# Kernel optimization log

Hardware: AMD Instinct MI355X
Metric: run time of the kernel (lower is better)

Reference implementation:

```python
import jax, jax.numpy as jnp
import numpy as np

DIM = 256
NUM_HEADS = 8
RATIO = 4
K_SAMPLES = 2
B, C, H, W = 2, 256, 64, 64


def setup_inputs() -> dict:
    key = jax.random.key(0)
    ks = jax.random.split(key, 12)
    N_low = (H // RATIO) * (W // RATIO)
    s = 0.02
    return {
        "q_high_feat": jax.random.normal(ks[0], (B, C, H, W), dtype=jnp.float32),
        "k_high_feat": jax.random.normal(ks[1], (B, C, H, W), dtype=jnp.float32),
        "v_high_feat": jax.random.normal(ks[2], (B, C, H, W), dtype=jnp.float32),
        "coarse_attn_map": jax.random.uniform(ks[3], (B, N_low, N_low), dtype=jnp.float32),
        "Wq": jax.random.normal(ks[4], (C, C), dtype=jnp.float32) * s,
        "bq": jnp.zeros((C,), dtype=jnp.float32),
        "Wk": jax.random.normal(ks[5], (C, C), dtype=jnp.float32) * s,
        "bk": jnp.zeros((C,), dtype=jnp.float32),
        "Wv": jax.random.normal(ks[6], (C, C), dtype=jnp.float32) * s,
        "bv": jnp.zeros((C,), dtype=jnp.float32),
        "Wo": jax.random.normal(ks[7], (C, C), dtype=jnp.float32) * s,
        "bo": jnp.zeros((C,), dtype=jnp.float32),
    }


def _sparse_indices(coarse_attn_map, H, W):
    # top-k coarse blocks per low-res query, expanded to high-res key indices
    H_low, W_low = H // RATIO, W // RATIO
    Bm, N_low, _ = coarse_attn_map.shape
    _, topk = jax.lax.top_k(coarse_attn_map, K_SAMPLES)          # (B, N_low, k)
    r0 = (topk // W_low) * RATIO                                  # top-left row
    c0 = (topk % W_low) * RATIO                                   # top-left col
    dr, dc = jnp.meshgrid(jnp.arange(RATIO), jnp.arange(RATIO), indexing='ij')
    dr, dc = dr.reshape(-1), dc.reshape(-1)                       # (ratio^2,)
    rows = r0[..., None] + dr                                     # (B, N_low, k, r2)
    cols = c0[..., None] + dc
    idx1d = (rows * W + cols).reshape(Bm, N_low, -1)              # (B, N_low, k*r2)
    # each low-res query row is repeated ratio^2 times (as in the torch code)
    return jnp.repeat(idx1d, RATIO * RATIO, axis=1)               # (B, N_high, K)


def reference(q_high_feat, k_high_feat, v_high_feat, coarse_attn_map,
              Wq, bq, Wk, bk, Wv, bv, Wo, bo):
    Bm, Cm, Hm, Wm = q_high_feat.shape
    N = Hm * Wm
    hd = Cm // NUM_HEADS
    scale = hd ** -0.5

    q_seq = q_high_feat.reshape(Bm, Cm, N).transpose(0, 2, 1)     # (B, N, C)
    k_seq = k_high_feat.reshape(Bm, Cm, N).transpose(0, 2, 1)
    v_seq = v_high_feat.reshape(Bm, Cm, N).transpose(0, 2, 1)

    final_idx = _sparse_indices(coarse_attn_map, Hm, Wm)          # (B, N, K)
    K_len = final_idx.shape[-1]

    q_proj = q_seq @ Wq + bq
    k_proj = k_seq @ Wk + bk
    v_proj = v_seq @ Wv + bv

    gather = jax.vmap(lambda p, i: p[i])                          # per-batch gather
    k_sp = gather(k_proj, final_idx)                              # (B, N, K, C)
    v_sp = gather(v_proj, final_idx)

    q = q_proj.reshape(Bm, N, NUM_HEADS, hd).transpose(0, 2, 1, 3)            # (B,h,N,d)
    k = k_sp.reshape(Bm, N, K_len, NUM_HEADS, hd).transpose(0, 3, 1, 2, 4)    # (B,h,N,K,d)
    v = v_sp.reshape(Bm, N, K_len, NUM_HEADS, hd).transpose(0, 3, 1, 2, 4)

    attn = jnp.einsum('bhnd,bhnkd->bhnk', q, k) * scale
    attn = jax.nn.softmax(attn, axis=-1)
    x = jnp.einsum('bhnk,bhnkd->bhnd', attn, v)
    x = x.transpose(0, 2, 1, 3).reshape(Bm, N, Cm)
    out = x @ Wo + bo
    return out.transpose(0, 2, 1).reshape(Bm, Cm, Hm, Wm)
```

## Files before the change

kernel.cpp:

```cpp
#include <hip/hip_runtime.h>
#include <hip/hip_bf16.h>
#include <cstddef>

#define BB 2
#define CC 256
#define HH 64
#define WW 64
#define NN 4096
#define NH 8
#define HD 32
#define NLOW 256
#define KLEN 32

typedef __attribute__((ext_vector_type(8))) short short8;
typedef __attribute__((ext_vector_type(4))) float float4v;

__device__ __forceinline__ float b2f(short s) {
    union { unsigned u; float f; } x;
    x.u = ((unsigned)(unsigned short)s) << 16;
    return x.f;
}
__device__ __forceinline__ short f2b(float f) {
    __hip_bfloat16 h = __float2bfloat16(f);
    return __builtin_bit_cast(short, h);
}

__device__ __forceinline__ void trans_tile(const float* __restrict__ src, size_t soff,
                                           int sld, short* __restrict__ dst,
                                           size_t doff, int dld) {
    __shared__ float tile[64 * 65];
    const int t = threadIdx.x;
    #pragma unroll
    for (int p = 0; p < 4; ++p) {
        int r  = p * 16 + (t >> 4);
        int c4 = (t & 15) * 4;
        float4v v = *(const float4v*)&src[soff + (size_t)r * sld + c4];
        tile[r * 65 + c4 + 0] = v[0];
        tile[r * 65 + c4 + 1] = v[1];
        tile[r * 65 + c4 + 2] = v[2];
        tile[r * 65 + c4 + 3] = v[3];
    }
    __syncthreads();
    #pragma unroll
    for (int p = 0; p < 2; ++p) {
        int n  = p * 32 + (t >> 3);
        int c0 = (t & 7) * 8;
        short8 o;
        #pragma unroll
        for (int j = 0; j < 8; ++j) o[j] = f2b(tile[(c0 + j) * 65 + n]);
        *(short8*)&dst[doff + (size_t)n * dld + c0] = o;
    }
}

__global__ __launch_bounds__(256) void prep_kernel(
    const float* __restrict__ q, const float* __restrict__ k,
    const float* __restrict__ v, const float* __restrict__ Wq,
    const float* __restrict__ Wk, const float* __restrict__ Wv,
    const float* __restrict__ Wo, const float* __restrict__ coarse,
    short* __restrict__ qt, short* __restrict__ kt, short* __restrict__ vt,
    short* __restrict__ Wt, int* __restrict__ fidx) {
    const int z = blockIdx.z;
    if (z < 6) {
        const float* src = (z < 2) ? q : (z < 4) ? k : v;
        short* dst       = (z < 2) ? qt : (z < 4) ? kt : vt;
        const int b = z & 1;
        const int n0 = blockIdx.x * 64, c0 = blockIdx.y * 64;
        trans_tile(src, (size_t)b * CC * NN + (size_t)c0 * NN + n0, NN,
                   dst, ((size_t)b * NN + n0) * CC + c0, CC);
        return;
    }
    const int id = blockIdx.y * 64 + blockIdx.x;
    if (id < 64) {
        const int wz = id >> 4, tile = id & 15;
        const float* src = (wz == 0) ? Wq : (wz == 1) ? Wk : (wz == 2) ? Wv : Wo;
        short* dst = Wt + (size_t)wz * CC * CC;
        const int co0 = (tile >> 2) * 64, ci0 = (tile & 3) * 64;
        trans_tile(src, (size_t)ci0 * CC + co0, CC,
                   dst, (size_t)co0 * CC + ci0, CC);
        return;
    }
    if (id >= 192) return;
    const int w = threadIdx.x >> 6, l = threadIdx.x & 63;
    const int row = (id - 64) * 4 + w;
    const float* r = coarse + (size_t)row * NLOW;
    float4v x = *(const float4v*)&r[l * 4];
    const int base = l * 4;
    float v1 = x[0]; int i1 = base;
    float v2 = x[1]; int i2 = base + 1;
    if (v2 > v1) { float tv = v1; v1 = v2; v2 = tv; int ti = i1; i1 = i2; i2 = ti; }
    #pragma unroll
    for (int j = 2; j < 4; ++j) {
        float e = x[j]; int ei = base + j;
        if (e > v1)      { v2 = v1; i2 = i1; v1 = e; i1 = ei; }
        else if (e > v2) { v2 = e;  i2 = ei; }
    }
    #pragma unroll
    for (int off = 1; off < 64; off <<= 1) {
        float ov1 = __shfl_xor(v1, off), ov2 = __shfl_xor(v2, off);
        int   oi1 = __shfl_xor(i1, off), oi2 = __shfl_xor(i2, off);
        bool aw = (v1 > ov1) || (v1 == ov1 && i1 < oi1);
        float nv1 = aw ? v1 : ov1;  int ni1 = aw ? i1 : oi1;
        float c1v = aw ? ov1 : v1;  int c1i = aw ? oi1 : i1;
        float c2v = aw ? v2 : ov2;  int c2i = aw ? i2 : oi2;
        bool bw = (c1v > c2v) || (c1v == c2v && c1i < c2i);
        v1 = nv1; i1 = ni1;
        v2 = bw ? c1v : c2v; i2 = bw ? c1i : c2i;
    }
    if (l < 32) {
        int s = l >> 4, jj = l & 15;
        int idx = s ? i2 : i1;
        int rr = jj >> 2, cc2 = jj & 3;
        fidx[(size_t)row * KLEN + l] =
            ((idx >> 4) * 4 + rr) * WW + (idx & 15) * 4 + cc2;
    }
}

template <int MT>
__device__ __forceinline__ void gemm_core(
    const short* __restrict__ A, int am0, const short* __restrict__ Bt, int bn0,
    short* As, short* Bs, float4v acc[MT][4]) {
    const int t = threadIdx.x;
    const int w = t >> 6, lane = t & 63;
    const int l16 = lane & 15, quad = lane >> 4;
    for (int k0 = 0; k0 < CC; k0 += 64) {
        __syncthreads();
        #pragma unroll
        for (int g = 0; g < 2 * MT; ++g) {
            int p = (w * 2 * MT + g) * 64 + lane;
            int m = p >> 3;
            int cl8 = (((p & 7) ^ (m & 7)) << 3);
            *(short8*)((char*)As + (size_t)p * 16) =
                *(const short8*)(A + (size_t)(am0 + m) * CC + k0 + cl8);
        }
        #pragma unroll
        for (int g = 0; g < 2; ++g) {
            int p = (w * 2 + g) * 64 + lane;
            int m = p >> 3;
            int cl8 = (((p & 7) ^ (m & 7)) << 3);
            *(short8*)((char*)Bs + (size_t)p * 16) =
                *(const short8*)(Bt + (size_t)(bn0 + m) * CC + k0 + cl8);
        }
        __syncthreads();
        #pragma unroll
        for (int s = 0; s < 2; ++s) {
            short8 bf[4];
            #pragma unroll
            for (int nt = 0; nt < 4; ++nt) {
                const int Rb = nt * 16 + l16;
                bf[nt] = *(const short8*)((const char*)Bs + Rb * 128 +
                                          (((s * 4 + quad) ^ (Rb & 7)) << 4));
            }
            #pragma unroll
            for (int mt = 0; mt < MT; ++mt) {
                const int Ra = mt * 64 + 16 * w + l16;
                short8 af = *(const short8*)((const char*)As + Ra * 128 +
                                             (((s * 4 + quad) ^ (Ra & 7)) << 4));
                #pragma unroll
                for (int nt = 0; nt < 4; ++nt)
                    acc[mt][nt] = __builtin_amdgcn_mfma_f32_16x16x32_bf16(
                        af, bf[nt], acc[mt][nt], 0, 0, 0);
            }
        }
    }
}

__global__ __launch_bounds__(256) void proj_gemm(
    const short* __restrict__ qt, const short* __restrict__ kt,
    const short* __restrict__ vt, const short* __restrict__ Wt,
    const float* __restrict__ bq, const float* __restrict__ bk,
    const float* __restrict__ bv,
    short* __restrict__ qp, short* __restrict__ kp, short* __restrict__ vp) {
    const int which = blockIdx.z;
    const short* A  = which == 0 ? qt : which == 1 ? kt : vt;
    const short* B  = Wt + (size_t)which * CC * CC;
    const float* bias = which == 0 ? bq : which == 1 ? bk : bv;
    short* outp     = which == 0 ? qp : which == 1 ? kp : vp;
    const int am0 = blockIdx.x * 128;
    const int nt0 = blockIdx.y * 64;

    __shared__ short As[128 * 64];
    __shared__ short Bs[64 * 64];
    float4v acc[2][4];
    #pragma unroll
    for (int i = 0; i < 2; ++i)
        #pragma unroll
        for (int j = 0; j < 4; ++j) acc[i][j] = (float4v)(0.f);

    gemm_core<2>(A, am0, B, nt0, As, Bs, acc);

    const int t = threadIdx.x;
    const int w = t >> 6, lane = t & 63;
    const int l16 = lane & 15, quad = lane >> 4;
    #pragma unroll
    for (int mt = 0; mt < 2; ++mt)
        #pragma unroll
        for (int nt = 0; nt < 4; ++nt) {
            int col = nt0 + nt * 16 + l16;
            float bv_ = bias[col];
            #pragma unroll
            for (int r = 0; r < 4; ++r) {
                int m = am0 + mt * 64 + 16 * w + quad * 4 + r;
                outp[(size_t)m * CC + col] = f2b(acc[mt][nt][r] + bv_);
            }
        }
}

#define KSTR 264

__global__ __launch_bounds__(256) void attn_kernel(
    const short* __restrict__ qp, const short* __restrict__ kp,
    const short* __restrict__ vp, const int* __restrict__ fidx,
    short* __restrict__ xo) {
    const int low = blockIdx.x, b = blockIdx.y;
    const int t = threadIdx.x;

    __shared__ short Ks[32 * KSTR];
    __shared__ short Vs[32 * KSTR];
    __shared__ int idx_s[KLEN];

    if (t < KLEN) {
        int idx = fidx[(size_t)(b * NLOW + low) * KLEN + t];
        idx_s[t] = idx < 0 ? 0 : (idx > NN - 1 ? NN - 1 : idx);
    }
    __syncthreads();

    const int* kpi = (const int*)kp;
    const int* vpi = (const int*)vp;
    const int half = t >> 7, col = t & 127;
    for (int j = 0; j < KLEN; j += 2) {
        int key = j + half;
        size_t base = (size_t)(b * NN + idx_s[key]) * (CC / 2);
        ((int*)&Ks[key * KSTR])[col] = kpi[base + col];
        ((int*)&Vs[key * KSTR])[col] = vpi[base + col];
    }
    __syncthreads();

    const int qi = t >> 4, h = (t >> 1) & 7, dh = t & 1;
    const int n = low * 16 + qi;
    const short* qrow = qp + (size_t)(b * NN + n) * CC + h * HD + dh * 16;

    float qv[16];
    #pragma unroll
    for (int c = 0; c < 2; ++c) {
        short8 v = *(const short8*)&qrow[c * 8];
        #pragma unroll
        for (int e = 0; e < 8; ++e) qv[c * 8 + e] = b2f(v[e]);
    }

    const float scale = 0.17677669529663687f;
    float sc[KLEN];
    for (int j = 0; j < KLEN; ++j) {
        const short* kr = &Ks[j * KSTR + h * HD + dh * 16];
        float s = 0.f;
        #pragma unroll
        for (int c = 0; c < 2; ++c) {
            short8 v = *(const short8*)&kr[c * 8];
            #pragma unroll
            for (int e = 0; e < 8; ++e) s += qv[c * 8 + e] * b2f(v[e]);
        }
        sc[j] = s;
    }
    float mx = -1e30f;
    #pragma unroll
    for (int j = 0; j < KLEN; ++j) {
        sc[j] = (sc[j] + __shfl_xor(sc[j], 1)) * scale;
        mx = fmaxf(mx, sc[j]);
    }
    float denom = 0.f;
    #pragma unroll
    for (int j = 0; j < KLEN; ++j) { sc[j] = __expf(sc[j] - mx); denom += sc[j]; }
    const float inv = 1.f / denom;

    float ov[16];
    #pragma unroll
    for (int d = 0; d < 16; ++d) ov[d] = 0.f;
    for (int j = 0; j < KLEN; ++j) {
        float p = sc[j] * inv;
        const short* vr = &Vs[j * KSTR + h * HD + dh * 16];
        #pragma unroll
        for (int c = 0; c < 2; ++c) {
            short8 v = *(const short8*)&vr[c * 8];
            #pragma unroll
            for (int e = 0; e < 8; ++e) ov[c * 8 + e] += p * b2f(v[e]);
        }
    }

    short* xrow = xo + (size_t)(b * NN + n) * CC + h * HD + dh * 16;
    #pragma unroll
    for (int c = 0; c < 2; ++c) {
        short8 v;
        #pragma unroll
        for (int e = 0; e < 8; ++e) v[e] = f2b(ov[c * 8 + e]);
        *(short8*)&xrow[c * 8] = v;
    }
}

__global__ __launch_bounds__(256) void outproj_gemm(
    const short* __restrict__ x, const short* __restrict__ Wto,
    const float* __restrict__ bo, float* __restrict__ out) {
    const int mt  = blockIdx.x;
    const int am0 = mt * 64;
    const int nt0 = blockIdx.y * 64;
    const int b   = mt >> 6;
    const int n0  = (mt & 63) * 64;

    __shared__ short As[64 * 64];
    __shared__ short Bs[64 * 64];
    __shared__ float Cs[64 * 65];

    float4v acc[1][4];
    #pragma unroll
    for (int j = 0; j < 4; ++j) acc[0][j] = (float4v)(0.f);

    gemm_core<1>(x, am0, Wto, nt0, As, Bs, acc);

    const int t = threadIdx.x;
    const int w = t >> 6, lane = t & 63;
    const int l16 = lane & 15, quad = lane >> 4;
    __syncthreads();
    #pragma unroll
    for (int nt = 0; nt < 4; ++nt) {
        float bias = bo[nt0 + nt * 16 + l16];
        #pragma unroll
        for (int r = 0; r < 4; ++r) {
            int m = 16 * w + quad * 4 + r;
            Cs[m * 65 + nt * 16 + l16] = acc[0][nt][r] + bias;
        }
    }
    __syncthreads();
    #pragma unroll
    for (int p = 0; p < 16; ++p) {
        int cl = (t >> 6) + 4 * p;
        int nl = t & 63;
        out[(size_t)(b * CC + nt0 + cl) * NN + n0 + nl] = Cs[nl * 65 + cl];
    }
}

extern "C" void kernel_launch(void* const* d_in, const int* in_sizes, int n_in,
                              void* d_out, int out_size, void* d_ws, size_t ws_size,
                              hipStream_t stream) {
    const float* q      = (const float*)d_in[0];
    const float* k      = (const float*)d_in[1];
    const float* v      = (const float*)d_in[2];
    const float* coarse = (const float*)d_in[3];
    const float* Wq     = (const float*)d_in[4];
    const float* bq     = (const float*)d_in[5];
    const float* Wk     = (const float*)d_in[6];
    const float* bk     = (const float*)d_in[7];
    const float* Wv     = (const float*)d_in[8];
    const float* bv     = (const float*)d_in[9];
    const float* Wo     = (const float*)d_in[10];
    const float* bo     = (const float*)d_in[11];

    char* ws = (char*)d_ws;
    const size_t MB4 = (size_t)BB * NN * CC * 2;
    short* qt = (short*)(ws);
    short* kt = (short*)(ws + MB4);
    short* vt = (short*)(ws + 2 * MB4);
    short* qp = (short*)(ws + 3 * MB4);
    short* kp = (short*)(ws + 4 * MB4);
    short* vp = (short*)(ws + 5 * MB4);
    short* Wt = (short*)(ws + 6 * MB4);
    int* fidx = (int*)(ws + 6 * MB4 + 4 * (size_t)CC * CC * 2);
    short* xo = qt;

    prep_kernel<<<dim3(64, 4, 7), 256, 0, stream>>>(q, k, v, Wq, Wk, Wv, Wo,
                                                    coarse, qt, kt, vt, Wt, fidx);
    proj_gemm<<<dim3(64, 4, 3), 256, 0, stream>>>(qt, kt, vt, Wt, bq, bk, bv,
                                                  qp, kp, vp);
    attn_kernel<<<dim3(NLOW, BB), 256, 0, stream>>>(qp, kp, vp, fidx, xo);
    outproj_gemm<<<dim3(128, 4), 256, 0, stream>>>(xo, Wt + 3 * CC * CC, bo,
                                                   (float*)d_out);
}
```

Before: 125.1 us.

## Fuse output projection into attention kernel via LDS-staged MFMA

The attention kernel no longer writes its per-head output to global memory. It stores the 16x256 bf16 tile for each low-res block into XOR-swizzled shared memory, then multiplies it by Wo with MFMA and writes the transposed fp32 output plus bias directly. This removes the separate output-projection launch and the round trip of the intermediate activation through global memory. The trade is that each block now reads the full Wo from global/L2 without LDS staging, which adds per-block weight traffic and some register pressure.

```diff
diff --git a/kernel.cpp b/kernel.cpp
--- a/kernel.cpp
+++ b/kernel.cpp
@@ -207,15 +207,17 @@
 
 #define KSTR 264
 
-__global__ __launch_bounds__(256) void attn_kernel(
+__global__ __launch_bounds__(256) void attn_out_kernel(
     const short* __restrict__ qp, const short* __restrict__ kp,
     const short* __restrict__ vp, const int* __restrict__ fidx,
-    short* __restrict__ xo) {
+    const short* __restrict__ Wto, const float* __restrict__ bo,
+    float* __restrict__ out) {
     const int low = blockIdx.x, b = blockIdx.y;
     const int t = threadIdx.x;
 
     __shared__ short Ks[32 * KSTR];
     __shared__ short Vs[32 * KSTR];
+    __shared__ short Xs[16 * 32 * 8];
     __shared__ int idx_s[KLEN];
 
     if (t < KLEN) {
@@ -285,54 +287,45 @@
         }
     }
 
-    short* xrow = xo + (size_t)(b * NN + n) * CC + h * HD + dh * 16;
     #pragma unroll
     for (int c = 0; c < 2; ++c) {
+        int lc = h * 4 + dh * 2 + c;
+        int p = qi * 32 + (lc & ~7) + ((lc & 7) ^ (qi & 7));
         short8 v;
         #pragma unroll
         for (int e = 0; e < 8; ++e) v[e] = f2b(ov[c * 8 + e]);
-        *(short8*)&xrow[c * 8] = v;
-    }
-}
-
-__global__ __launch_bounds__(256) void outproj_gemm(
-    const short* __restrict__ x, const short* __restrict__ Wto,
-    const float* __restrict__ bo, float* __restrict__ out) {
-    const int mt  = blockIdx.x;
-    const int am0 = mt * 64;
-    const int nt0 = blockIdx.y * 64;
-    const int b   = mt >> 6;
-    const int n0  = (mt & 63) * 64;
-
-    __shared__ short As[64 * 64];
-    __shared__ short Bs[64 * 64];
-    __shared__ float Cs[64 * 65];
-
-    float4v acc[1][4];
-    #pragma unroll
-    for (int j = 0; j < 4; ++j) acc[0][j] = (float4v)(0.f);
-
-    gemm_core<1>(x, am0, Wto, nt0, As, Bs, acc);
-
-    const int t = threadIdx.x;
+        *(short8*)((char*)Xs + (size_t)p * 16) = v;
+    }
+    __syncthreads();
+
     const int w = t >> 6, lane = t & 63;
     const int l16 = lane & 15, quad = lane >> 4;
-    __syncthreads();
+    float4v acc[4];
+    #pragma unroll
+    for (int i = 0; i < 4; ++i) acc[i] = (float4v)(0.f);
+
+    #pragma unroll
+    for (int s = 0; s < 8; ++s) {
+        int lc = s * 4 + quad;
+        int p = l16 * 32 + (lc & ~7) + ((lc & 7) ^ (l16 & 7));
+        short8 af = *(const short8*)((const char*)Xs + (size_t)p * 16);
+        #pragma unroll
+        for (int nt = 0; nt < 4; ++nt) {
+            int co = w * 64 + nt * 16 + l16;
+            short8 bf = *(const short8*)(Wto + (size_t)co * CC + s * 32 + quad * 8);
+            acc[nt] = __builtin_amdgcn_mfma_f32_16x16x32_bf16(af, bf, acc[nt], 0, 0, 0);
+        }
+    }
+
+    const int nbase = low * 16 + quad * 4;
     #pragma unroll
     for (int nt = 0; nt < 4; ++nt) {
-        float bias = bo[nt0 + nt * 16 + l16];
-        #pragma unroll
-        for (int r = 0; r < 4; ++r) {
-            int m = 16 * w + quad * 4 + r;
-            Cs[m * 65 + nt * 16 + l16] = acc[0][nt][r] + bias;
-        }
-    }
-    __syncthreads();
-    #pragma unroll
-    for (int p = 0; p < 16; ++p) {
-        int cl = (t >> 6) + 4 * p;
-        int nl = t & 63;
-        out[(size_t)(b * CC + nt0 + cl) * NN + n0 + nl] = Cs[nl * 65 + cl];
+        int c = w * 64 + nt * 16 + l16;
+        float bias = bo[c];
+        float4v o;
+        #pragma unroll
+        for (int r = 0; r < 4; ++r) o[r] = acc[nt][r] + bias;
+        *(float4v*)&out[(size_t)(b * CC + c) * NN + nbase] = o;
     }
 }
 
@@ -362,13 +355,12 @@
     short* vp = (short*)(ws + 5 * MB4);
     short* Wt = (short*)(ws + 6 * MB4);
     int* fidx = (int*)(ws + 6 * MB4 + 4 * (size_t)CC * CC * 2);
-    short* xo = qt;
 
     prep_kernel<<<dim3(64, 4, 7), 256, 0, stream>>>(q, k, v, Wq, Wk, Wv, Wo,
                                                     coarse, qt, kt, vt, Wt, fidx);
     proj_gemm<<<dim3(64, 4, 3), 256, 0, stream>>>(qt, kt, vt, Wt, bq, bk, bv,
                                                   qp, kp, vp);
-    attn_kernel<<<dim3(NLOW, BB), 256, 0, stream>>>(qp, kp, vp, fidx, xo);
-    outproj_gemm<<<dim3(128, 4), 256, 0, stream>>>(xo, Wt + 3 * CC * CC, bo,
-                                                   (float*)d_out);
-}
+    attn_out_kernel<<<dim3(NLOW, BB), 256, 0, stream>>>(qp, kp, vp, fidx,
+                                                        Wt + 3 * CC * CC, bo,
+                                                        (float*)d_out);
+}
```

After: 120.3 us (median of 2 runs). -3.9%, faster.
